# Kernel optimization log

Hardware: AMD Instinct MI355X
Metric: run time of the kernel (lower is better)

Reference implementation:

```python
import jax, jax.numpy as jnp
import numpy as np

L_MAX = 3
N_MAX = 8
N_PSEUDO = 4
N_SPECIES = 4
CUTOFF = 5.0


def real_sph_harm(u):
    # u: [E,3] unit vectors -> real spherical harmonics, l=0..3, [E,16]
    x, y, z = u[:, 0], u[:, 1], u[:, 2]
    x2, y2, z2 = x * x, y * y, z * z
    Y = [
        0.28209479177387814 * jnp.ones_like(x),
        0.4886025119029199 * y,
        0.4886025119029199 * z,
        0.4886025119029199 * x,
        1.0925484305920792 * x * y,
        1.0925484305920792 * y * z,
        0.31539156525252005 * (3.0 * z2 - 1.0),
        1.0925484305920792 * x * z,
        0.5462742152960396 * (x2 - y2),
        0.5900435899266435 * y * (3.0 * x2 - y2),
        2.890611442640554 * x * y * z,
        0.4570457994644658 * y * (5.0 * z2 - 1.0),
        0.3731763325901154 * z * (5.0 * z2 - 3.0),
        0.4570457994644658 * x * (5.0 * z2 - 1.0),
        1.445305721320277 * z * (x2 - y2),
        0.5900435899266435 * x * (x2 - 3.0 * y2),
    ]
    return jnp.stack(Y, axis=-1)


def setup_inputs() -> dict:
    key = jax.random.key(0)
    k0, k1, k2, k3 = jax.random.split(key, 4)
    N, E = 20000, 320000
    positions = jax.random.normal(k0, (N, 3), jnp.float32) * 2.0
    cells = (30.0 * jnp.eye(3, dtype=jnp.float32))[None]  # [1,3,3]
    species = jax.random.randint(k1, (N,), 0, N_SPECIES)  # species indices
    edge_indices = jax.random.randint(k2, (2, E), 0, N)
    edge_shifts = jnp.zeros((E, 3), jnp.int32)
    species_embed = jax.random.normal(k3, (N_SPECIES, N_PSEUDO), jnp.float32)  # alchemical coupling
    radial_mu = jnp.linspace(0.0, CUTOFF, N_MAX).astype(jnp.float32)
    radial_sigma = jnp.full((1,), 0.6, jnp.float32)
    return {
        "positions": positions,
        "cells": cells,
        "species": species,
        "edge_indices": edge_indices,
        "edge_shifts": edge_shifts,
        "species_embed": species_embed,
        "radial_mu": radial_mu,
        "radial_sigma": radial_sigma,
    }


def reference(positions, cells, species, edge_indices, edge_shifts, species_embed, radial_mu, radial_sigma):
    i, j = edge_indices[0], edge_indices[1]
    # per-edge displacement with periodic shifts
    rij = positions[j] - positions[i] + edge_shifts.astype(positions.dtype) @ cells[0]  # [E,3]
    r = jnp.sqrt(jnp.sum(rij * rij, axis=-1) + 1e-12)  # [E]
    u = rij / r[:, None]
    # smooth cosine cutoff
    fcut = jnp.where(r < CUTOFF, 0.5 * (jnp.cos(jnp.pi * r / CUTOFF) + 1.0), 0.0)
    # radial expansion [E, n_max]
    sig = radial_sigma[0]
    R = jnp.exp(-((r[:, None] - radial_mu) ** 2) / (2.0 * sig * sig)) * fcut[:, None]
    # angular expansion [E, (l_max+1)^2]
    Y = real_sph_harm(u)
    # alchemical pseudo-species embedding of the neighbor species [E, P]
    ej = species_embed[species[j]]
    N = positions.shape[0]
    outs = []
    for l in range(L_MAX + 1):
        Yl = Y[:, l * l:(l + 1) * (l + 1)]  # [E, 2l+1]
        # per-edge spherical-expansion contribution, properties = (pseudo, n) flattened -> Q
        feat = jnp.einsum('em,ep,en->empn', Yl, ej, R).reshape(Yl.shape[0], 2 * l + 1, -1)
        # scatter edges to centers: c_{i,m,q}
        c = jax.ops.segment_sum(feat, i, num_segments=N)  # [N, 2l+1, Q]
        cg = (2 * l + 1) ** (-0.5)
        # power spectrum: cg * sum_m c_{imq} c_{imr}  -> [N, Q, Q]
        ps = cg * jnp.einsum('nmq,nmr->nqr', c, c)
        outs.append(ps.reshape(N, -1))
    return jnp.concatenate(outs, axis=-1)  # [N, sum_l Q^2] = [20000, 4096]
```

## Files before the change

kernel.cpp:

```cpp
#include <hip/hip_runtime.h>
#include <math.h>

#define NM       16
#define NQ       32
#define CUT      5.0f
#define CAP      96

typedef float v4f __attribute__((ext_vector_type(4)));

__global__ __launch_bounds__(256) void edge_bin_kernel(
    const float* __restrict__ pos,
    const float* __restrict__ cells,
    const int*   __restrict__ species,
    const int*   __restrict__ eidx,
    const int*   __restrict__ eshift,
    int*         __restrict__ counts,
    float4*      __restrict__ buckets,
    int E)
{
    const int e = blockIdx.x * blockDim.x + threadIdx.x;
    if (e >= E) return;

    const int i = eidx[e];
    const int j = eidx[E + e];

    float dx = pos[3 * j + 0] - pos[3 * i + 0];
    float dy = pos[3 * j + 1] - pos[3 * i + 1];
    float dz = pos[3 * j + 2] - pos[3 * i + 2];

    const int sx = eshift[3 * e + 0];
    const int sy = eshift[3 * e + 1];
    const int sz = eshift[3 * e + 2];
    dx += (float)sx * cells[0] + (float)sy * cells[3] + (float)sz * cells[6];
    dy += (float)sx * cells[1] + (float)sy * cells[4] + (float)sz * cells[7];
    dz += (float)sx * cells[2] + (float)sy * cells[5] + (float)sz * cells[8];

    const float r2 = dx * dx + dy * dy + dz * dz;
    if (r2 >= CUT * CUT) return;

    const int slot = atomicAdd(&counts[i], 1);
    if (slot < CAP)
        buckets[(size_t)i * CAP + slot] =
            make_float4(dx, dy, dz, __int_as_float(species[j]));
}

__global__ __launch_bounds__(256) void node_fused_kernel(
    const float4* __restrict__ buckets,
    const int*    __restrict__ counts,
    const float*  __restrict__ semb,
    const float*  __restrict__ mu,
    const float*  __restrict__ sigma,
    float*        __restrict__ out,
    int N)
{
    const int node = blockIdx.x;
    const int tid  = threadIdx.x;

    __shared__ float sY[64][17];
    __shared__ float sW[64][33];
    __shared__ __align__(16) float sc[NM * NQ];
    __shared__ float s_mu[8];
    __shared__ float s_semb[16];

    if (tid < 8)  s_mu[tid]   = mu[tid];
    if (tid < 16) s_semb[tid] = semb[tid];

    const float sig    = sigma[0];
    const float inv2s2 = -1.0f / (2.0f * sig * sig);

    const int cnt = min(counts[node], CAP);

    const int q  = tid & 31;
    const int m0 = tid >> 5;
    float acc0 = 0.0f, acc1 = 0.0f;

    for (int base = 0; base < cnt; base += 64) {
        const int nb = min(cnt - base, 64);
        __syncthreads();

        const int lane = tid & 63;
        const int half = tid >> 6;
        if (lane < nb && half < 2) {
            const float4 b = buckets[(size_t)node * CAP + base + lane];
            const float dx = b.x, dy = b.y, dz = b.z;
            const float r2 = dx * dx + dy * dy + dz * dz + 1e-12f;
            const float r  = sqrtf(r2);
            const float invr = 1.0f / r;
            if (half == 0) {
                const float x = dx * invr, y = dy * invr, z = dz * invr;
                const float x2 = x * x, y2 = y * y, z2 = z * z;
                float* Yr = sY[lane];
                Yr[0]  = 0.28209479177387814f;
                Yr[1]  = 0.4886025119029199f * y;
                Yr[2]  = 0.4886025119029199f * z;
                Yr[3]  = 0.4886025119029199f * x;
                Yr[4]  = 1.0925484305920792f * x * y;
                Yr[5]  = 1.0925484305920792f * y * z;
                Yr[6]  = 0.31539156525252005f * (3.0f * z2 - 1.0f);
                Yr[7]  = 1.0925484305920792f * x * z;
                Yr[8]  = 0.5462742152960396f * (x2 - y2);
                Yr[9]  = 0.5900435899266435f * y * (3.0f * x2 - y2);
                Yr[10] = 2.890611442640554f  * x * y * z;
                Yr[11] = 0.4570457994644658f * y * (5.0f * z2 - 1.0f);
                Yr[12] = 0.3731763325901154f * z * (5.0f * z2 - 3.0f);
                Yr[13] = 0.4570457994644658f * x * (5.0f * z2 - 1.0f);
                Yr[14] = 1.445305721320277f  * z * (x2 - y2);
                Yr[15] = 0.5900435899266435f * x * (x2 - 3.0f * y2);
            } else {
                const float fcut = 0.5f * (__cosf(0.62831853071795864f * r) + 1.0f);
                const int sj = __float_as_int(b.w);
                float R[8];
#pragma unroll
                for (int n = 0; n < 8; ++n) {
                    const float dr = r - s_mu[n];
                    R[n] = __expf(dr * dr * inv2s2) * fcut;
                }
                float* Wr = sW[lane];
#pragma unroll
                for (int p = 0; p < 4; ++p) {
                    const float ejp = s_semb[sj * 4 + p];
#pragma unroll
                    for (int n = 0; n < 8; ++n)
                        Wr[p * 8 + n] = ejp * R[n];
                }
            }
        }
        __syncthreads();

        for (int e = 0; e < nb; ++e) {
            const float w = sW[e][q];
            acc0 += sY[e][m0]     * w;
            acc1 += sY[e][m0 + 8] * w;
        }
    }

    __syncthreads();
    sc[m0 * NQ + q]       = acc0;
    sc[(m0 + 8) * NQ + q] = acc1;
    __syncthreads();

    const float cg[4] = {1.0f, 0.57735026918962576f,
                         0.44721359549995794f, 0.37796447300922723f};
    const int qc = tid >> 3;
    const int r8 = tid & 7;

    const v4f* sc4 = (const v4f*)sc;
    v4f* op = (v4f*)out + (size_t)node * 1024;

#pragma unroll
    for (int l = 0; l < 4; ++l) {
        const int mb = l * l;
        const int mc = 2 * l + 1;
        v4f s = {0.0f, 0.0f, 0.0f, 0.0f};
        for (int m = 0; m < mc; ++m) {
            const float a  = sc[(mb + m) * NQ + qc];
            const v4f   bv = sc4[(mb + m) * 8 + r8];
            s += a * bv;
        }
        s *= cg[l];
        __builtin_nontemporal_store(s, &op[l * 256 + tid]);
    }
}

extern "C" void kernel_launch(void* const* d_in, const int* in_sizes, int n_in,
                              void* d_out, int out_size, void* d_ws, size_t ws_size,
                              hipStream_t stream) {
    const float* pos     = (const float*)d_in[0];
    const float* cells   = (const float*)d_in[1];
    const int*   species = (const int*)  d_in[2];
    const int*   eidx    = (const int*)  d_in[3];
    const int*   eshift  = (const int*)  d_in[4];
    const float* semb    = (const float*)d_in[5];
    const float* mu      = (const float*)d_in[6];
    const float* sigma   = (const float*)d_in[7];
    float*       out     = (float*)d_out;

    const int N = in_sizes[0] / 3;
    const int E = in_sizes[3] / 2;

    float4* buckets = (float4*)d_ws;
    const size_t bucket_bytes = (size_t)N * CAP * sizeof(float4);
    int* counts = (int*)((char*)d_ws + bucket_bytes);

    hipMemsetAsync(counts, 0, (size_t)N * sizeof(int), stream);

    edge_bin_kernel<<<(E + 255) / 256, 256, 0, stream>>>(
        pos, cells, species, eidx, eshift, counts, buckets, E);

    node_fused_kernel<<<N, 256, 0, stream>>>(
        buckets, counts, semb, mu, sigma, out, N);
}
```

Measured before the change: 359.2 us.

## Map one node per wavefront with XOR-swizzled LDS tiles, dropping block barriers

```diff
diff --git a/kernel.cpp b/kernel.cpp
--- a/kernel.cpp
+++ b/kernel.cpp
@@ -5,6 +5,8 @@
 #define NQ       32
 #define CUT      5.0f
 #define CAP      96
+#define TS       32
+#define GPB      4
 
 typedef float v4f __attribute__((ext_vector_type(4)));
 
@@ -44,7 +46,7 @@
             make_float4(dx, dy, dz, __int_as_float(species[j]));
 }
 
-__global__ __launch_bounds__(256) void node_fused_kernel(
+__global__ __launch_bounds__(256, 4) void node_fused_kernel(
     const float4* __restrict__ buckets,
     const int*    __restrict__ counts,
     const float*  __restrict__ semb,
@@ -53,112 +55,134 @@
     float*        __restrict__ out,
     int N)
 {
-    const int node = blockIdx.x;
     const int tid  = threadIdx.x;
-
-    __shared__ float sY[64][17];
-    __shared__ float sW[64][33];
-    __shared__ __align__(16) float sc[NM * NQ];
-    __shared__ float s_mu[8];
-    __shared__ float s_semb[16];
-
-    if (tid < 8)  s_mu[tid]   = mu[tid];
-    if (tid < 16) s_semb[tid] = semb[tid];
+    const int lane = tid & 63;
+    const int wv   = tid >> 6;
+    const int node = blockIdx.x * GPB + wv;
+
+    __shared__ __align__(16) float sT[GPB][TS * 48];
+    __shared__ __align__(16) float sC[GPB][NM * NQ];
+
+    if (node >= N) return;
 
     const float sig    = sigma[0];
     const float inv2s2 = -1.0f / (2.0f * sig * sig);
 
     const int cnt = min(counts[node], CAP);
 
-    const int q  = tid & 31;
-    const int m0 = tid >> 5;
-    float acc0 = 0.0f, acc1 = 0.0f;
-
-    for (int base = 0; base < cnt; base += 64) {
-        const int nb = min(cnt - base, 64);
-        __syncthreads();
-
-        const int lane = tid & 63;
-        const int half = tid >> 6;
-        if (lane < nb && half < 2) {
+    const int m   = lane >> 2;
+    const int p4  = lane & 3;
+    const int cw0 = p4 * 2;
+
+    v4f acc0 = {0.f, 0.f, 0.f, 0.f};
+    v4f acc1 = {0.f, 0.f, 0.f, 0.f};
+
+    float* const tile = &sT[wv][0];
+
+    for (int base = 0; base < cnt; base += TS) {
+        const int nb = min(cnt - base, TS);
+
+        asm volatile("s_waitcnt lgkmcnt(0)" ::: "memory");
+        __builtin_amdgcn_sched_barrier(0);
+
+        if (lane < nb) {
             const float4 b = buckets[(size_t)node * CAP + base + lane];
             const float dx = b.x, dy = b.y, dz = b.z;
             const float r2 = dx * dx + dy * dy + dz * dz + 1e-12f;
             const float r  = sqrtf(r2);
             const float invr = 1.0f / r;
-            if (half == 0) {
-                const float x = dx * invr, y = dy * invr, z = dz * invr;
-                const float x2 = x * x, y2 = y * y, z2 = z * z;
-                float* Yr = sY[lane];
-                Yr[0]  = 0.28209479177387814f;
-                Yr[1]  = 0.4886025119029199f * y;
-                Yr[2]  = 0.4886025119029199f * z;
-                Yr[3]  = 0.4886025119029199f * x;
-                Yr[4]  = 1.0925484305920792f * x * y;
-                Yr[5]  = 1.0925484305920792f * y * z;
-                Yr[6]  = 0.31539156525252005f * (3.0f * z2 - 1.0f);
-                Yr[7]  = 1.0925484305920792f * x * z;
-                Yr[8]  = 0.5462742152960396f * (x2 - y2);
-                Yr[9]  = 0.5900435899266435f * y * (3.0f * x2 - y2);
-                Yr[10] = 2.890611442640554f  * x * y * z;
-                Yr[11] = 0.4570457994644658f * y * (5.0f * z2 - 1.0f);
-                Yr[12] = 0.3731763325901154f * z * (5.0f * z2 - 3.0f);
-                Yr[13] = 0.4570457994644658f * x * (5.0f * z2 - 1.0f);
-                Yr[14] = 1.445305721320277f  * z * (x2 - y2);
-                Yr[15] = 0.5900435899266435f * x * (x2 - 3.0f * y2);
-            } else {
-                const float fcut = 0.5f * (__cosf(0.62831853071795864f * r) + 1.0f);
-                const int sj = __float_as_int(b.w);
-                float R[8];
+            const float x = dx * invr, y = dy * invr, z = dz * invr;
+            const float x2 = x * x, y2 = y * y, z2 = z * z;
+
+            v4f* rowY = (v4f*)&tile[lane * 48];
+            v4f y0 = {0.28209479177387814f,
+                      0.4886025119029199f * y,
+                      0.4886025119029199f * z,
+                      0.4886025119029199f * x};
+            v4f y1 = {1.0925484305920792f * x * y,
+                      1.0925484305920792f * y * z,
+                      0.31539156525252005f * (3.0f * z2 - 1.0f),
+                      1.0925484305920792f * x * z};
+            v4f y2v = {0.5462742152960396f * (x2 - y2),
+                       0.5900435899266435f * y * (3.0f * x2 - y2),
+                       2.890611442640554f  * x * y * z,
+                       0.4570457994644658f * y * (5.0f * z2 - 1.0f)};
+            v4f y3 = {0.3731763325901154f * z * (5.0f * z2 - 3.0f),
+                      0.4570457994644658f * x * (5.0f * z2 - 1.0f),
+                      1.445305721320277f  * z * (x2 - y2),
+                      0.5900435899266435f * x * (x2 - 3.0f * y2)};
+            rowY[0] = y0; rowY[1] = y1; rowY[2] = y2v; rowY[3] = y3;
+
+            const float fcut = 0.5f * (__cosf(0.62831853071795864f * r) + 1.0f);
+            const int sj = __float_as_int(b.w);
+            const v4f ej = ((const v4f*)semb)[sj];
+
+            float R[8];
 #pragma unroll
-                for (int n = 0; n < 8; ++n) {
-                    const float dr = r - s_mu[n];
-                    R[n] = __expf(dr * dr * inv2s2) * fcut;
-                }
-                float* Wr = sW[lane];
-#pragma unroll
-                for (int p = 0; p < 4; ++p) {
-                    const float ejp = s_semb[sj * 4 + p];
-#pragma unroll
-                    for (int n = 0; n < 8; ++n)
-                        Wr[p * 8 + n] = ejp * R[n];
-                }
+            for (int n = 0; n < 8; ++n) {
+                const float dr = r - mu[n];
+                R[n] = __expf(dr * dr * inv2s2) * fcut;
             }
+            const v4f rlo = {R[0], R[1], R[2], R[3]};
+            const v4f rhi = {R[4], R[5], R[6], R[7]};
+
+            v4f* rowW = (v4f*)&tile[lane * 48 + 16];
+            const int sw = lane & 7;
+            rowW[(0) ^ sw] = ej[0] * rlo; rowW[(1) ^ sw] = ej[0] * rhi;
+            rowW[(2) ^ sw] = ej[1] * rlo; rowW[(3) ^ sw] = ej[1] * rhi;
+            rowW[(4) ^ sw] = ej[2] * rlo; rowW[(5) ^ sw] = ej[2] * rhi;
+            rowW[(6) ^ sw] = ej[3] * rlo; rowW[(7) ^ sw] = ej[3] * rhi;
         }
-        __syncthreads();
+
+        asm volatile("s_waitcnt lgkmcnt(0)" ::: "memory");
+        __builtin_amdgcn_sched_barrier(0);
 
         for (int e = 0; e < nb; ++e) {
-            const float w = sW[e][q];
-            acc0 += sY[e][m0]     * w;
-            acc1 += sY[e][m0 + 8] * w;
+            const float* rowp = &tile[e * 48];
+            const float ym = rowp[m];
+            const int es = e & 7;
+            const v4f wlo = ((const v4f*)(rowp + 16))[(cw0)     ^ es];
+            const v4f whi = ((const v4f*)(rowp + 16))[(cw0 + 1) ^ es];
+            acc0 += ym * wlo;
+            acc1 += ym * whi;
         }
     }
 
-    __syncthreads();
-    sc[m0 * NQ + q]       = acc0;
-    sc[(m0 + 8) * NQ + q] = acc1;
-    __syncthreads();
+    float* const cw_ = &sC[wv][0];
+    ((v4f*)cw_)[m * 8 + ((cw0)     ^ (m & 7))] = acc0;
+    ((v4f*)cw_)[m * 8 + ((cw0 + 1) ^ (m & 7))] = acc1;
+    asm volatile("s_waitcnt lgkmcnt(0)" ::: "memory");
+    __builtin_amdgcn_sched_barrier(0);
 
     const float cg[4] = {1.0f, 0.57735026918962576f,
                          0.44721359549995794f, 0.37796447300922723f};
-    const int qc = tid >> 3;
-    const int r8 = tid & 7;
-
-    const v4f* sc4 = (const v4f*)sc;
+    const int qt = lane >> 3;
+    const int rt = lane & 7;
+
     v4f* op = (v4f*)out + (size_t)node * 1024;
 
 #pragma unroll
     for (int l = 0; l < 4; ++l) {
         const int mb = l * l;
         const int mc = 2 * l + 1;
-        v4f s = {0.0f, 0.0f, 0.0f, 0.0f};
-        for (int m = 0; m < mc; ++m) {
-            const float a  = sc[(mb + m) * NQ + qc];
-            const v4f   bv = sc4[(mb + m) * 8 + r8];
-            s += a * bv;
+        v4f s0 = {0.f,0.f,0.f,0.f}, s1 = {0.f,0.f,0.f,0.f};
+        v4f s2 = {0.f,0.f,0.f,0.f}, s3 = {0.f,0.f,0.f,0.f};
+        for (int mm = 0; mm < mc; ++mm) {
+            const int row = mb + mm;
+            const v4f* crow4 = (const v4f*)cw_ + row * 8;
+            const int rs = row & 7;
+            const v4f qv = crow4[qt ^ rs];
+            const v4f rv = crow4[rt ^ rs];
+            s0 += qv[0] * rv;
+            s1 += qv[1] * rv;
+            s2 += qv[2] * rv;
+            s3 += qv[3] * rv;
         }
-        s *= cg[l];
-        __builtin_nontemporal_store(s, &op[l * 256 + tid]);
+        const float g = cg[l];
+        __builtin_nontemporal_store(s0 * g, &op[l * 256 + (qt * 4 + 0) * 8 + rt]);
+        __builtin_nontemporal_store(s1 * g, &op[l * 256 + (qt * 4 + 1) * 8 + rt]);
+        __builtin_nontemporal_store(s2 * g, &op[l * 256 + (qt * 4 + 2) * 8 + rt]);
+        __builtin_nontemporal_store(s3 * g, &op[l * 256 + (qt * 4 + 3) * 8 + rt]);
     }
 }
 
@@ -187,6 +211,6 @@
     edge_bin_kernel<<<(E + 255) / 256, 256, 0, stream>>>(
         pos, cells, species, eidx, eshift, counts, buckets, E);
 
-    node_fused_kernel<<<N, 256, 0, stream>>>(
+    node_fused_kernel<<<(N + GPB - 1) / GPB, 256, 0, stream>>>(
         buckets, counts, semb, mu, sigma, out, N);
 }
```

After: 366.7 us. +2.1%, slower.
